# Optimization experiments

Measured on AMD Instinct MI355X. Metric: run time of the kernel, lower is better.

Reference implementation:

```python
import jax, jax.numpy as jnp
import numpy as np

NUM_TAGS = 9
INNER_DIM = 64
HIDDEN = 768
MASK_VAL = 1e12


def setup_inputs() -> dict:
    key = jax.random.key(0)
    k1, k2, k3, k4 = jax.random.split(key, 4)
    B, S = 16, 512
    encoder_output = jax.random.normal(k1, (B, S, HIDDEN), dtype=jnp.float32)
    token_ids = jax.random.randint(k2, (B, S), 0, 30000, dtype=jnp.int64)
    attention_mask = jnp.ones((B, S), dtype=jnp.int32)
    W = jax.random.normal(k3, (HIDDEN, NUM_TAGS * INNER_DIM * 2), dtype=jnp.float32) * 0.02
    b = jax.random.normal(k4, (NUM_TAGS * INNER_DIM * 2,), dtype=jnp.float32) * 0.02
    return {"encoder_output": encoder_output, "token_ids": token_ids,
            "attention_mask": attention_mask, "W": W, "b": b}


def _rope_sin_cos(seq_len, dim, dtype):
    # sinusoidal position embedding, interleaved then repeat_interleave(2)
    pos = jnp.arange(seq_len, dtype=dtype)[:, None]              # [S,1]
    inv = jnp.power(10000.0, -2.0 * jnp.arange(dim // 2, dtype=dtype) / dim)
    ang = pos * inv                                              # [S,d/2]
    sin = jnp.repeat(jnp.sin(ang), 2, axis=-1)                   # [S,d]
    cos = jnp.repeat(jnp.cos(ang), 2, axis=-1)                   # [S,d]
    return sin, cos


def _rotate_half(x):
    # stack([-x[...,1::2], x[...,::2]], -1).reshape(x.shape)
    x2 = jnp.stack([-x[..., 1::2], x[..., ::2]], axis=-1)
    return x2.reshape(x.shape)


def reference(encoder_output, token_ids, attention_mask, W, b):
    B, S, _ = encoder_output.shape
    d = INNER_DIM
    out = encoder_output @ W + b                                 # [B,S,T*2d]
    out = out.reshape(B, S, NUM_TAGS, 2 * d)
    qw, kw = out[..., :d], out[..., d:]                          # [B,S,T,d]

    sin, cos = _rope_sin_cos(S, d, encoder_output.dtype)
    sin = sin[None, :, None, :]                                  # [1,S,1,d]
    cos = cos[None, :, None, :]
    qw = qw * cos + _rotate_half(qw) * sin
    kw = kw * cos + _rotate_half(kw) * sin

    logits = jnp.einsum('bshd,bthd->bhst', qw, kw)               # [B,T,S,S]

    pad = attention_mask.astype(logits.dtype)[:, None, None, :]  # key-side mask
    logits = logits * pad - (1.0 - pad) * MASK_VAL
    tril = jnp.tril(jnp.ones((S, S), dtype=logits.dtype), -1)
    logits = logits - tril * MASK_VAL
    return logits / jnp.sqrt(jnp.asarray(d, logits.dtype))
```

## Files before the change

### kernel.cpp

```cpp
#include <hip/hip_runtime.h>

#define MASK_VALF 1000000000000.0f

typedef __attribute__((ext_vector_type(8))) short s16x8;
typedef __attribute__((ext_vector_type(4))) float f32x4;

__device__ __forceinline__ unsigned f2bf_u(float f) {
    union { float f; unsigned u; } v; v.f = f;
    return (v.u + 0x7FFFu + ((v.u >> 16) & 1u)) >> 16;
}
__device__ __forceinline__ short f2bf(float f) { return (short)(f2bf_u(f) & 0xFFFFu); }

#define GLOAD16(gp, lp) __builtin_amdgcn_global_load_lds( \
    (const __attribute__((address_space(1))) void*)(gp),  \
    (__attribute__((address_space(3))) void*)(lp), 16, 0, 0)

__global__ __launch_bounds__(256) void prep_all(
    const float* __restrict__ enc, short* __restrict__ encb,
    const float* __restrict__ W, short* __restrict__ wtb,
    float* __restrict__ scf)
{
    const int blk = blockIdx.x;
    const int t = threadIdx.x;
    if (blk < 6144) {
        int i = blk * 256 + t;
        float4 v = ((const float4*)enc)[i];
        short4 o;
        o.x = f2bf(v.x); o.y = f2bf(v.y); o.z = f2bf(v.z); o.w = f2bf(v.w);
        ((short4*)encb)[i] = o;
    } else if (blk < 7008) {
        __shared__ float tile[32][33];
        int tb = blk - 6144;
        int tbx = tb % 36;
        int tby = tb / 36;
        int tx = t & 31, ty = t >> 5;
#pragma unroll
        for (int r = 0; r < 4; ++r) {
            int row = ty + r * 8;
            tile[row][tx] = W[(tby * 32 + row) * 1152 + tbx * 32 + tx];
        }
        __syncthreads();
#pragma unroll
        for (int r = 0; r < 4; ++r) {
            int row = ty + r * 8;
            wtb[(size_t)(tbx * 32 + row) * 768 + tby * 32 + tx] = f2bf(tile[tx][row]);
        }
    } else {
        int id = (blk - 7008) * 256 + t;
        int pos = id >> 5, j = id & 31;
        float inv = powf(10000.0f, -2.0f * (float)j / 64.0f);
        float ang = (float)pos * inv;
        float s, c;
        sincosf(ang, &s, &c);
        scf[id * 2]     = c;
        scf[id * 2 + 1] = s;
    }
}

__global__ __launch_bounds__(256) void gemm1_rope(
    const short* __restrict__ A,
    const short* __restrict__ Bt,
    const float* __restrict__ bias,
    const float* __restrict__ scf,
    short* __restrict__ qk)
{
    __shared__ __align__(16) short As[128 * 32];
    __shared__ __align__(16) short Bs[128 * 32];
    const int t = threadIdx.x;
    const int w = t >> 6, lane = t & 63;
    const int lr = lane & 15, quad = lane >> 4;
    const int wm = w >> 1, wn = w & 1;
    const int m0 = blockIdx.y * 128;
    const int n0 = blockIdx.x * 128;

    f32x4 acc[4][4] = {};

    const short* gA = A  + (size_t)(m0 + (t >> 2)) * 768 + (t & 3) * 8;
    const short* gB = Bt + (size_t)(n0 + (t >> 2)) * 768 + (t & 3) * 8;
    short* lA0 = &As[w * 512];
    short* lA1 = &As[2048 + w * 512];
    short* lB0 = &Bs[w * 512];
    short* lB1 = &Bs[2048 + w * 512];

    for (int kt = 0; kt < 24; ++kt) {
        __syncthreads();
        GLOAD16(gA,            lA0);
        GLOAD16(gA + 64 * 768, lA1);
        GLOAD16(gB,            lB0);
        GLOAD16(gB + 64 * 768, lB1);
        gA += 32; gB += 32;
        __syncthreads();

        s16x8 af[4], bw[4];
#pragma unroll
        for (int i = 0; i < 4; ++i)
            af[i] = *(const s16x8*)&Bs[(wm * 64 + i * 16 + lr) * 32 + quad * 8];
#pragma unroll
        for (int j = 0; j < 4; ++j)
            bw[j] = *(const s16x8*)&As[(wn * 64 + j * 16 + lr) * 32 + quad * 8];
#pragma unroll
        for (int i = 0; i < 4; ++i)
#pragma unroll
            for (int j = 0; j < 4; ++j)
                acc[i][j] = __builtin_amdgcn_mfma_f32_16x16x32_bf16(af[i], bw[j], acc[i][j], 0, 0, 0);
    }

#pragma unroll
    for (int i = 0; i < 4; ++i) {
        const int colg0 = n0 + wm * 64 + i * 16 + quad * 4;
        const float4 bv = *(const float4*)&bias[colg0];
        const int tag = colg0 >> 7;
        const int qkf = (colg0 >> 6) & 1;
        const int dd0 = colg0 & 63;
        const int jj0 = dd0 >> 1;
        short* qbase = qk + ((size_t)tag * 2 + qkf) * 512 * 64 + dd0;
#pragma unroll
        for (int j = 0; j < 4; ++j) {
            const int rowg = m0 + wn * 64 + j * 16 + lr;
            const int bidx = rowg >> 9;
            const int pos  = rowg & 511;
            const float4 cs = *(const float4*)&scf[pos * 64 + jj0 * 2];
            float x0 = acc[i][j][0] + bv.x;
            float x1 = acc[i][j][1] + bv.y;
            float x2 = acc[i][j][2] + bv.z;
            float x3 = acc[i][j][3] + bv.w;
            float o0 = x0 * cs.x - x1 * cs.y;
            float o1 = x1 * cs.x + x0 * cs.y;
            float o2 = x2 * cs.z - x3 * cs.w;
            float o3 = x3 * cs.z + x2 * cs.w;
            int2 st;
            st.x = (int)(f2bf_u(o0) & 0xFFFFu) | (int)(f2bf_u(o1) << 16);
            st.y = (int)(f2bf_u(o2) & 0xFFFFu) | (int)(f2bf_u(o3) << 16);
            *(int2*)&qbase[((size_t)bidx * 9 * 2 * 512 + pos) * 64] = st;
        }
    }
}

__global__ __launch_bounds__(256) void gemm2_mask(
    const short* __restrict__ qk,
    const int* __restrict__ amask,
    float* __restrict__ out)
{
    const int t = threadIdx.x;
    const int w = t >> 6, lane = t & 63;
    const int lr = lane & 15, quad = lane >> 4;
    const int wm = w >> 1, wn = w & 1;
    const int bh = blockIdx.z;
    const int bidx = bh / 9;
    const int s0 = blockIdx.y * 128;
    const int t0 = blockIdx.x * 128;

    const short* qbase = qk + (size_t)bh * 2 * 512 * 64;
    const short* kbase = qbase + 512 * 64;

    const short* kf = kbase + (size_t)(t0 + wm * 64 + lr) * 64 + quad * 8;
    const short* qf = qbase + (size_t)(s0 + wn * 64 + lr) * 64 + quad * 8;

    f32x4 acc[4][4] = {};
#pragma unroll
    for (int kk = 0; kk < 64; kk += 32) {
        s16x8 af[4], bw[4];
#pragma unroll
        for (int i = 0; i < 4; ++i)
            af[i] = *(const s16x8*)&kf[i * 16 * 64 + kk];
#pragma unroll
        for (int j = 0; j < 4; ++j)
            bw[j] = *(const s16x8*)&qf[j * 16 * 64 + kk];
#pragma unroll
        for (int i = 0; i < 4; ++i)
#pragma unroll
            for (int j = 0; j < 4; ++j)
                acc[i][j] = __builtin_amdgcn_mfma_f32_16x16x32_bf16(af[i], bw[j], acc[i][j], 0, 0, 0);
    }

#pragma unroll
    for (int i = 0; i < 4; ++i) {
        const int tg0 = t0 + wm * 64 + i * 16 + quad * 4;
        const int4 am = *(const int4*)&amask[bidx * 512 + tg0];
        const float4 pad = make_float4((float)am.x, (float)am.y, (float)am.z, (float)am.w);
        const float4 mk = make_float4((1.0f - pad.x) * MASK_VALF, (1.0f - pad.y) * MASK_VALF,
                                      (1.0f - pad.z) * MASK_VALF, (1.0f - pad.w) * MASK_VALF);
#pragma unroll
        for (int j = 0; j < 4; ++j) {
            const int sg = s0 + wn * 64 + j * 16 + lr;
            f32x4 v;
            v[0] = (acc[i][j][0] * pad.x - mk.x - (sg > tg0     ? MASK_VALF : 0.0f)) * 0.125f;
            v[1] = (acc[i][j][1] * pad.y - mk.y - (sg > tg0 + 1 ? MASK_VALF : 0.0f)) * 0.125f;
            v[2] = (acc[i][j][2] * pad.z - mk.z - (sg > tg0 + 2 ? MASK_VALF : 0.0f)) * 0.125f;
            v[3] = (acc[i][j][3] * pad.w - mk.w - (sg > tg0 + 3 ? MASK_VALF : 0.0f)) * 0.125f;
            __builtin_nontemporal_store(v, (f32x4*)&out[((size_t)bh * 512 + sg) * 512 + tg0]);
        }
    }
}

extern "C" void kernel_launch(void* const* d_in, const int* in_sizes, int n_in,
                              void* d_out, int out_size, void* d_ws, size_t ws_size,
                              hipStream_t stream) {
    const float* enc   = (const float*)d_in[0];
    const int*   amask = (const int*)d_in[2];
    const float* W     = (const float*)d_in[3];
    const float* bias  = (const float*)d_in[4];
    float* out = (float*)d_out;

    char* ws = (char*)d_ws;
    short* encb = (short*)(ws);
    short* wtb  = (short*)(ws + 12582912);
    float* scf  = (float*)(ws + 14352384);
    short* qk   = (short*)(ws + 14483456);

    prep_all  <<<7072, 256, 0, stream>>>(enc, encb, W, wtb, scf);
    gemm1_rope<<<dim3(9, 64), 256, 0, stream>>>(encb, wtb, bias, scf, qk);
    gemm2_mask<<<dim3(4, 4, 144), 256, 0, stream>>>(qk, amask, out);
}
```

Baseline: 229.5 us.

## Double-buffer LDS tiles in gemm1 and swizzle block order for L2 reuse

```diff
diff --git a/kernel.cpp b/kernel.cpp
--- a/kernel.cpp
+++ b/kernel.cpp
@@ -64,45 +64,52 @@
     const float* __restrict__ scf,
     short* __restrict__ qk)
 {
-    __shared__ __align__(16) short As[128 * 32];
-    __shared__ __align__(16) short Bs[128 * 32];
+    __shared__ __align__(16) short As[2][128 * 32];
+    __shared__ __align__(16) short Bs[2][128 * 32];
     const int t = threadIdx.x;
     const int w = t >> 6, lane = t & 63;
     const int lr = lane & 15, quad = lane >> 4;
     const int wm = w >> 1, wn = w & 1;
-    const int m0 = blockIdx.y * 128;
-    const int n0 = blockIdx.x * 128;
+
+    const int lin = blockIdx.y * 9 + blockIdx.x;
+    const int swz = (lin & 7) * 72 + (lin >> 3);
+    const int n0 = (swz % 9) * 128;
+    const int m0 = (swz / 9) * 128;
 
     f32x4 acc[4][4] = {};
 
     const short* gA = A  + (size_t)(m0 + (t >> 2)) * 768 + (t & 3) * 8;
     const short* gB = Bt + (size_t)(n0 + (t >> 2)) * 768 + (t & 3) * 8;
-    short* lA0 = &As[w * 512];
-    short* lA1 = &As[2048 + w * 512];
-    short* lB0 = &Bs[w * 512];
-    short* lB1 = &Bs[2048 + w * 512];
+
+    GLOAD16(gA,            &As[0][w * 512]);
+    GLOAD16(gA + 64 * 768, &As[0][2048 + w * 512]);
+    GLOAD16(gB,            &Bs[0][w * 512]);
+    GLOAD16(gB + 64 * 768, &Bs[0][2048 + w * 512]);
+    gA += 32; gB += 32;
+    __syncthreads();
 
     for (int kt = 0; kt < 24; ++kt) {
-        __syncthreads();
-        GLOAD16(gA,            lA0);
-        GLOAD16(gA + 64 * 768, lA1);
-        GLOAD16(gB,            lB0);
-        GLOAD16(gB + 64 * 768, lB1);
-        gA += 32; gB += 32;
-        __syncthreads();
-
+        const int cur = kt & 1, nxt = cur ^ 1;
+        if (kt < 23) {
+            GLOAD16(gA,            &As[nxt][w * 512]);
+            GLOAD16(gA + 64 * 768, &As[nxt][2048 + w * 512]);
+            GLOAD16(gB,            &Bs[nxt][w * 512]);
+            GLOAD16(gB + 64 * 768, &Bs[nxt][2048 + w * 512]);
+            gA += 32; gB += 32;
+        }
         s16x8 af[4], bw[4];
 #pragma unroll
         for (int i = 0; i < 4; ++i)
-            af[i] = *(const s16x8*)&Bs[(wm * 64 + i * 16 + lr) * 32 + quad * 8];
+            af[i] = *(const s16x8*)&Bs[cur][(wm * 64 + i * 16 + lr) * 32 + quad * 8];
 #pragma unroll
         for (int j = 0; j < 4; ++j)
-            bw[j] = *(const s16x8*)&As[(wn * 64 + j * 16 + lr) * 32 + quad * 8];
+            bw[j] = *(const s16x8*)&As[cur][(wn * 64 + j * 16 + lr) * 32 + quad * 8];
 #pragma unroll
         for (int i = 0; i < 4; ++i)
 #pragma unroll
             for (int j = 0; j < 4; ++j)
                 acc[i][j] = __builtin_amdgcn_mfma_f32_16x16x32_bf16(af[i], bw[j], acc[i][j], 0, 0, 0);
+        __syncthreads();
     }
 
 #pragma unroll
```

Result: slower. 234.7 us (+2.3%).
